# Kernel tuning notes

Measured on AMD Instinct MI355X. Metric: run time of the kernel, lower is better.

Reference implementation:

```python
import jax, jax.numpy as jnp
import numpy as np
from jax import lax

DN = ('NCHW', 'OIHW', 'NCHW')

def conv(x, w, b):
    y = lax.conv_general_dilated(x, w, (1, 1), 'SAME', dimension_numbers=DN)
    return y + b[None, :, None, None]


def setup_inputs() -> dict:
    key = jax.random.key(0)
    ks = jax.random.split(key, 32)
    B, C, H, W = 16, 256, 40, 100
    dim, N, kd, ncls, mdim = 134, 4, 128, 2, 256
    inc = C + 2
    s = 0.05  # weight init scale
    def w(k, shape):
        return jax.random.normal(k, shape, jnp.float32) * s
    d = {}
    d['features'] = jax.random.normal(ks[0], (B, C, H, W), jnp.float32)
    d['iw0'] = w(ks[1], (dim, inc, 3, 3)); d['ib0'] = jnp.zeros((dim,), jnp.float32)
    d['iw1'] = w(ks[2], (dim, dim, 3, 3)); d['ib1'] = jnp.zeros((dim,), jnp.float32)
    d['iw2'] = w(ks[3], (dim, dim, 3, 3)); d['ib2'] = jnp.zeros((dim,), jnp.float32)
    d['iw3'] = w(ks[4], (dim, dim, 3, 3)); d['ib3'] = jnp.zeros((dim,), jnp.float32)
    d['iam_w'] = w(ks[5], (N, dim, 3, 3)); d['iam_b'] = jnp.zeros((N,), jnp.float32)
    d['cls_w'] = w(ks[6], (ncls, dim));    d['cls_b'] = jnp.zeros((ncls,), jnp.float32)
    d['mk_w'] = w(ks[7], (kd, dim));       d['mk_b'] = jnp.zeros((kd,), jnp.float32)
    d['mw0'] = w(ks[8], (mdim, inc, 3, 3));  d['mb0'] = jnp.zeros((mdim,), jnp.float32)
    d['mw1'] = w(ks[9], (mdim, mdim, 3, 3)); d['mb1'] = jnp.zeros((mdim,), jnp.float32)
    d['mw2'] = w(ks[10], (mdim, mdim, 3, 3)); d['mb2'] = jnp.zeros((mdim,), jnp.float32)
    d['mw3'] = w(ks[11], (mdim, mdim, 3, 3)); d['mb3'] = jnp.zeros((mdim,), jnp.float32)
    d['pw'] = w(ks[12], (kd, mdim, 1, 1));   d['pb'] = jnp.zeros((kd,), jnp.float32)
    return d


def reference(features, iw0, ib0, iw1, ib1, iw2, ib2, iw3, ib3, iam_w, iam_b,
              cls_w, cls_b, mk_w, mk_b, mw0, mb0, mw1, mb1, mw2, mb2, mw3, mb3, pw, pb):
    B, C, H, W = features.shape
    # coordinate channels in [-1, 1]
    y_loc = -1.0 + 2.0 * jnp.arange(H, dtype=jnp.float32) / (H - 1)
    x_loc = -1.0 + 2.0 * jnp.arange(W, dtype=jnp.float32) / (W - 1)
    yy, xx = jnp.meshgrid(y_loc, x_loc, indexing='ij')  # [H,W]
    coords = jnp.broadcast_to(jnp.stack([xx, yy], 0)[None], (B, 2, H, W))
    feat = jnp.concatenate([coords, features], axis=1)  # [B, C+2, H, W]

    # instance branch conv stack (258 -> 134, relu)
    f = jax.nn.relu(conv(feat, iw0, ib0))
    f = jax.nn.relu(conv(f, iw1, ib1))
    f = jax.nn.relu(conv(f, iw2, ib2))
    f = jax.nn.relu(conv(f, iw3, ib3))  # [B,134,H,W]

    params = jnp.transpose(f, (0, 2, 3, 1)).reshape(-1, 134)  # [B*H*W, 134]

    iam = conv(f, iam_w, iam_b)           # [B,N,H,W]
    iam_prob = jax.nn.sigmoid(iam)
    Bn, Ni = iam_prob.shape[:2]

    # seed extraction: per-map flat argmax (pos = r*W + c, label always 0 in original)
    pos = jnp.argmax(iam_prob.reshape(Bn * Ni, H * W), axis=-1)  # [B*N], values in [0, H*W)
    sel = params[pos]                     # gather rows (indexes batch-0 region, as in source)
    mask_params = sel[:, :67]
    reg_params = sel[:, 67:]

    # iam-weighted pooling
    ip = iam_prob.reshape(Bn, Ni, H * W)
    ip = ip / jnp.clip(ip.sum(-1, keepdims=True), 1e-6)
    inst = jnp.einsum('bnl,bcl->bnc', ip, f.reshape(Bn, 134, H * W))  # [B,N,134]

    pred_logits = inst @ cls_w.T + cls_b  # [B,N,2]
    pred_kernel = inst @ mk_w.T + mk_b    # [B,N,128]

    # mask branch (258 -> 256 x4 relu, then 1x1 projection to 128, no relu)
    m = jax.nn.relu(conv(feat, mw0, mb0))
    m = jax.nn.relu(conv(m, mw1, mb1))
    m = jax.nn.relu(conv(m, mw2, mb2))
    m = jax.nn.relu(conv(m, mw3, mb3))
    mf = conv(m, pw, pb)                  # [B,128,H,W]

    pred_masks = jnp.einsum('bnk,bkl->bnl', pred_kernel, mf.reshape(Bn, 128, H * W))
    pred_masks = pred_masks.reshape(Bn * Ni, H, W)
    pred_logits = pred_logits.reshape(Bn * Ni, -1)
    return pred_logits, mask_params, reg_params, pred_masks
```

## Files before the change

kernel.cpp:

```cpp
#include <hip/hip_runtime.h>
#include <hip/hip_bf16.h>
#include <math.h>

constexpr int HW = 4000;
constexpr int HP = 4284;
constexpr int HPAD = 4480;
constexpr int NPIXH = 16 * HP;

typedef short s16x8 __attribute__((ext_vector_type(8)));
typedef float f32x4 __attribute__((ext_vector_type(4)));
typedef unsigned short u16x4 __attribute__((ext_vector_type(4)));
typedef unsigned short u16;

__device__ __forceinline__ u16 f2bf(float f) {
    __hip_bfloat16 h = __float2bfloat16(f);
    u16 b; __builtin_memcpy(&b, &h, 2); return b;
}
__device__ __forceinline__ float bf2f(u16 b) {
    __hip_bfloat16 h; __builtin_memcpy(&h, &b, 2); return __bfloat162float(h);
}

__device__ __forceinline__ void gload_lds16(const void* g, void* l) {
    __builtin_amdgcn_global_load_lds(
        (const __attribute__((address_space(1))) void*)g,
        (__attribute__((address_space(3))) void*)l, 16, 0, 0);
}

__global__ __launch_bounds__(256) void repack_w(
    const float* __restrict__ W, u16* __restrict__ Wh, u16* __restrict__ Wl,
    int Cout, int Cin, int NRS, int nCh, int Npad, int do_lo)
{
    const int chunk = blockIdx.x * 256 + threadIdx.x;
    const int per = Npad * 4;
    const int total = NRS * nCh * per;
    if (chunk >= total) return;
    const int q = chunk % per;
    const int t2 = chunk / per;
    const int ch = t2 % nCh;
    const int rs = t2 / nCh;
    const int f = q >> 6, g = (q >> 4) & 3, rA = q & 15;
    const int n = f * 16 + rA;
    u16x4 hp[2], lp[2];
    #pragma unroll
    for (int j = 0; j < 8; ++j) {
        const int c = ch * 32 + g * 8 + j;
        const float v = (n < Cout && c < Cin) ? W[((size_t)n * Cin + c) * NRS + rs] : 0.f;
        const u16 hb = f2bf(v);
        hp[j >> 2][j & 3] = hb;
        lp[j >> 2][j & 3] = f2bf(v - bf2f(hb));
    }
    const size_t o = (size_t)chunk * 8;
    *(u16x4*)(Wh + o) = hp[0]; *(u16x4*)(Wh + o + 4) = hp[1];
    if (do_lo) { *(u16x4*)(Wl + o) = lp[0]; *(u16x4*)(Wl + o + 4) = lp[1]; }
}

__global__ __launch_bounds__(256) void prep_x0(
    const float* __restrict__ feat, u16* __restrict__ Xh, u16* __restrict__ Xl)
{
    const int p = blockIdx.x * 256 + threadIdx.x;
    if (p >= NPIXH) return;
    const int b = p / HP; const int rem = p - b * HP;
    const int hh = rem / 102, wp = rem - hh * 102;
    const bool halo = (hh == 0) | (hh == 41) | (wp == 0) | (wp == 101);
    const int h = hh - 1, w = wp - 1;
    const int hw = h * 100 + w;
    const float xw = -1.f + 2.f * (float)w / 99.f;
    const float yh = -1.f + 2.f * (float)h / 39.f;
    for (int g = 0; g < 36; ++g) {
        u16x4 hp[2], lp[2];
        #pragma unroll
        for (int j = 0; j < 8; ++j) {
            const int c = g * 8 + j;
            float v = 0.f;
            if (!halo) {
                if (c == 0) v = xw;
                else if (c == 1) v = yh;
                else if (c < 258) v = feat[((size_t)(b * 256 + (c - 2))) * HW + hw];
            }
            const u16 hb = f2bf(v);
            hp[j >> 2][j & 3] = hb;
            lp[j >> 2][j & 3] = f2bf(v - bf2f(hb));
        }
        const size_t o = ((size_t)(b * 36 + g) * HPAD + rem) * 8;
        *(u16x4*)(Xh + o) = hp[0]; *(u16x4*)(Xh + o + 4) = hp[1];
        *(u16x4*)(Xl + o) = lp[0]; *(u16x4*)(Xl + o + 4) = lp[1];
    }
}

__global__ __launch_bounds__(256) void zero_halo_pl(
    u16* __restrict__ pa, u16* __restrict__ pb, int nGa, int nGb)
{
    const int p = blockIdx.x * 256 + threadIdx.x;
    if (p >= NPIXH) return;
    const int b = p / HP; const int rem = p - b * HP;
    const int hh = rem / 102, wp = rem - hh * 102;
    if (!((hh == 0) | (hh == 41) | (wp == 0) | (wp == 101))) return;
    const u16x4 z = {0, 0, 0, 0};
    for (int g = 0; g < nGa; ++g) {
        const size_t o = ((size_t)(b * nGa + g) * HPAD + rem) * 8;
        *(u16x4*)(pa + o) = z; *(u16x4*)(pa + o + 4) = z;
    }
    if (pb)
        for (int g = 0; g < nGb; ++g) {
            const size_t o = ((size_t)(b * nGb + g) * HPAD + rem) * 8;
            *(u16x4*)(pb + o) = z; *(u16x4*)(pb + o + 4) = z;
        }
}

template <int SPLIT, int BN, int NRS, int OUTMODE>
__global__ __launch_bounds__(256) void conv_mfma(
    const u16* __restrict__ Xhi, const u16* __restrict__ Xlo,
    const u16* __restrict__ Whi, const u16* __restrict__ Wlo,
    const float* __restrict__ bias,
    u16* __restrict__ Yhi, u16* __restrict__ Ylo, float* __restrict__ Yf,
    int nCh, int Npad, int Cout, int CoutStore, int nGout, int do_relu)
{
    constexpr int FW = BN / 32;
    constexpr int PS = 384;
    constexpr int NIW = (BN * 4) / 256;

    __shared__ u16 lsXh[4 * PS * 8];
    __shared__ u16 lsXl[SPLIT == 3 ? 4 * PS * 8 : 8];
    __shared__ u16 lsWh[2][BN * 32];
    __shared__ u16 lsWl[2][SPLIT == 3 ? BN * 32 : 8];

    const int tid = threadIdx.x, lane = tid & 63, wid = tid >> 6;
    const int b = blockIdx.z;
    const int off = blockIdx.y * 128;
    const int n0 = blockIdx.x * BN;
    const int nGin = nCh * 4;
    const int h0 = off / 100, w0 = off - h0 * 100;
    const int pTL0 = h0 * 102 + w0;

    const int wn = (wid & 1) * (BN / 2);
    const int wm = (wid >> 1) * 64;
    const int gA = lane >> 4, rA = lane & 15;

    int pd[4]; bool mval[4];
    #pragma unroll
    for (int fb = 0; fb < 4; ++fb) {
        int mm = off + wm + fb * 16 + rA;
        mval[fb] = mm < HW;
        if (!mval[fb]) mm = HW - 1;
        const int h = mm / 100, w = mm - h * 100;
        pd[fb] = (h * 102 + w) - pTL0;
    }

    auto stageX = [&](int ch) {
        const size_t src = ((size_t)(b * nGin + ch * 4 + wid) * HPAD + pTL0) * 8;
        const int dst = wid * PS * 8;
        #pragma unroll
        for (int i = 0; i < 6; ++i) {
            gload_lds16(Xhi + src + (size_t)(i * 64 + lane) * 8,
                        (char*)lsXh + (dst + i * 64 * 8) * 2);
            if constexpr (SPLIT == 3)
                gload_lds16(Xlo + src + (size_t)(i * 64 + lane) * 8,
                            (char*)lsXl + (dst + i * 64 * 8) * 2);
        }
    };
    auto stageW = [&](int ch, int rs, int buf) {
        const size_t wb = ((size_t)(rs * nCh + ch) * (Npad * 4) + (n0 >> 4) * 64) * 8;
        #pragma unroll
        for (int i = 0; i < NIW; ++i) {
            const int q = tid + i * 256;
            gload_lds16(Whi + wb + (size_t)q * 8, (char*)&lsWh[buf][0] + (q & ~63) * 16);
            if constexpr (SPLIT == 3)
                gload_lds16(Wlo + wb + (size_t)q * 8, (char*)&lsWl[buf][0] + (q & ~63) * 16);
        }
    };

    f32x4 acc[FW][4];
    #pragma unroll
    for (int i = 0; i < FW; ++i)
        #pragma unroll
        for (int j = 0; j < 4; ++j) acc[i][j] = (f32x4){0.f, 0.f, 0.f, 0.f};

    for (int ch = 0; ch < nCh; ++ch) {
        stageX(ch);
        stageW(ch, 0, 0);
        __syncthreads();
        for (int rs = 0; rs < NRS; ++rs) {
            if (rs + 1 < NRS) stageW(ch, rs + 1, (rs + 1) & 1);
            const int cb = rs & 1;
            const int toff = (NRS == 9) ? ((rs / 3) * 102 + (rs - 3 * (rs / 3))) : 103;

            s16x8 aW[FW], bX[4];
            s16x8 aWl[SPLIT == 3 ? FW : 1], bXl[SPLIT == 3 ? 4 : 1];
            #pragma unroll
            for (int fa = 0; fa < FW; ++fa) {
                const int idx = (((wn >> 4) + fa) * 64 + lane) * 8;
                aW[fa] = *(const s16x8*)&lsWh[cb][idx];
                if constexpr (SPLIT == 3) aWl[fa] = *(const s16x8*)&lsWl[cb][idx];
            }
            #pragma unroll
            for (int fb = 0; fb < 4; ++fb) {
                const int xi = (gA * PS + pd[fb] + toff) * 8;
                bX[fb] = *(const s16x8*)&lsXh[xi];
                if constexpr (SPLIT == 3) bXl[fb] = *(const s16x8*)&lsXl[xi];
            }
            #pragma unroll
            for (int fa = 0; fa < FW; ++fa)
                #pragma unroll
                for (int fb = 0; fb < 4; ++fb) {
                    acc[fa][fb] = __builtin_amdgcn_mfma_f32_16x16x32_bf16(
                        aW[fa], bX[fb], acc[fa][fb], 0, 0, 0);
                    if constexpr (SPLIT == 3) {
                        acc[fa][fb] = __builtin_amdgcn_mfma_f32_16x16x32_bf16(
                            aW[fa], bXl[fb], acc[fa][fb], 0, 0, 0);
                        acc[fa][fb] = __builtin_amdgcn_mfma_f32_16x16x32_bf16(
                            aWl[fa], bX[fb], acc[fa][fb], 0, 0, 0);
                    }
                }
            __syncthreads();
        }
    }

    #pragma unroll
    for (int fb = 0; fb < 4; ++fb) {
        if (!mval[fb]) continue;
        const int mm = off + wm + fb * 16 + rA;
        #pragma unroll
        for (int fa = 0; fa < FW; ++fa) {
            const int nb = n0 + wn + fa * 16 + gA * 4;
            if (nb >= CoutStore) continue;
            f32x4 v = acc[fa][fb];
            #pragma unroll
            for (int i = 0; i < 4; ++i) {
                const int n = nb + i;
                float x = (n < Cout) ? (v[i] + bias[n]) : 0.f;
                if (do_relu) x = fmaxf(x, 0.f);
                v[i] = x;
            }
            if constexpr (OUTMODE == 2) {
                *(f32x4*)(Yf + (size_t)(b * HW + mm) * CoutStore + nb) = v;
            } else {
                const size_t o =
                    ((size_t)(b * nGout + (nb >> 3)) * HPAD + pTL0 + pd[fb] + 103) * 8 + (nb & 7);
                u16x4 hp;
                #pragma unroll
                for (int i = 0; i < 4; ++i) hp[i] = f2bf(v[i]);
                *(u16x4*)(Yhi + o) = hp;
                if constexpr (OUTMODE == 0) {
                    u16x4 lp;
                    #pragma unroll
                    for (int i = 0; i < 4; ++i) lp[i] = f2bf(v[i] - bf2f(hp[i]));
                    *(u16x4*)(Ylo + o) = lp;
                }
            }
        }
    }
}

__global__ __launch_bounds__(256) void iam_conv_nhwc(
    const u16* __restrict__ fhi, const u16* __restrict__ flo,
    const float* __restrict__ Wt, const float* __restrict__ bias,
    float* __restrict__ iam)
{
    __shared__ float wsm[9 * 134 * 4];
    const int tid = threadIdx.x;
    for (int i = tid; i < 4824; i += 256) {
        const int rs = i / 536; const int rem = i - rs * 536;
        const int c = rem >> 2; const int n = rem & 3;
        wsm[i] = Wt[(n * 134 + c) * 9 + rs];
    }
    __syncthreads();
    const int m = blockIdx.x * 256 + tid;
    const int b = m / HW; const int hw = m - b * HW;
    const int h = hw / 100, w = hw - h * 100;
    const int pTL = h * 102 + w;
    float a0 = bias[0], a1 = bias[1], a2 = bias[2], a3 = bias[3];
    for (int rs = 0; rs < 9; ++rs) {
        const int pA = pTL + (rs / 3) * 102 + (rs % 3);
        const float* wrow = &wsm[rs * 536];
        for (int g = 0; g < 17; ++g) {
            const size_t o = ((size_t)(b * 20 + g) * HPAD + pA) * 8;
            s16x8 hv = *(const s16x8*)(fhi + o);
            s16x8 lv = *(const s16x8*)(flo + o);
            #pragma unroll
            for (int j = 0; j < 8; ++j) {
                const int c = g * 8 + j;
                if (c < 134) {
                    const float v = bf2f((u16)hv[j]) + bf2f((u16)lv[j]);
                    const float* wc = wrow + c * 4;
                    a0 = fmaf(v, wc[0], a0); a1 = fmaf(v, wc[1], a1);
                    a2 = fmaf(v, wc[2], a2); a3 = fmaf(v, wc[3], a3);
                }
            }
        }
    }
    iam[(b * 4 + 0) * HW + hw] = a0;
    iam[(b * 4 + 1) * HW + hw] = a1;
    iam[(b * 4 + 2) * HW + hw] = a2;
    iam[(b * 4 + 3) * HW + hw] = a3;
}

__device__ __forceinline__ float sigmoidf_dev(float x) {
    return 1.f / (1.f + expf(-x));
}

__global__ __launch_bounds__(256) void stats_kernel(
    const float* __restrict__ iam, int* __restrict__ pos, float* __restrict__ denom)
{
    const int i = blockIdx.x;
    const int tid = threadIdx.x;
    const float* p = &iam[i * HW];
    float bm = -1e30f; int bi = 0; float sum = 0.f;
    for (int l = tid; l < HW; l += 256) {
        const float s = sigmoidf_dev(p[l]);
        sum += s;
        if (s > bm) { bm = s; bi = l; }
    }
    __shared__ float sm[256]; __shared__ int si[256]; __shared__ float ss[256];
    sm[tid] = bm; si[tid] = bi; ss[tid] = sum;
    __syncthreads();
    for (int off = 128; off > 0; off >>= 1) {
        if (tid < off) {
            ss[tid] += ss[tid + off];
            const float m2 = sm[tid + off]; const int i2 = si[tid + off];
            if (m2 > sm[tid] || (m2 == sm[tid] && i2 < si[tid])) { sm[tid] = m2; si[tid] = i2; }
        }
        __syncthreads();
    }
    if (tid == 0) { pos[i] = si[0]; denom[i] = fmaxf(ss[0], 1e-6f); }
}

__global__ __launch_bounds__(256) void inst_nhwc(
    const u16* __restrict__ fhi, const u16* __restrict__ flo,
    const float* __restrict__ iam, const float* __restrict__ denom,
    float* __restrict__ inst)
{
    const int b = blockIdx.x, g = blockIdx.y;
    const int tid = threadIdx.x;
    float acc[4][8] = {};
    const size_t pbase = (size_t)(b * 20 + g) * HPAD;
    for (int l = tid; l < HW; l += 256) {
        const int p = (l / 100 + 1) * 102 + (l % 100) + 1;
        s16x8 hv = *(const s16x8*)(fhi + (pbase + p) * 8);
        s16x8 lv = *(const s16x8*)(flo + (pbase + p) * 8);
        float fv[8];
        #pragma unroll
        for (int j = 0; j < 8; ++j) fv[j] = bf2f((u16)hv[j]) + bf2f((u16)lv[j]);
        #pragma unroll
        for (int n = 0; n < 4; ++n) {
            const float s = sigmoidf_dev(iam[(b * 4 + n) * HW + l]);
            #pragma unroll
            for (int j = 0; j < 8; ++j) acc[n][j] = fmaf(s, fv[j], acc[n][j]);
        }
    }
    __shared__ float red[128];
    const int lane = tid & 63, wid = tid >> 6;
    #pragma unroll
    for (int n = 0; n < 4; ++n)
        #pragma unroll
        for (int j = 0; j < 8; ++j) {
            float v = acc[n][j];
            #pragma unroll
            for (int off = 32; off > 0; off >>= 1) v += __shfl_xor(v, off);
            if (lane == 0) red[wid * 32 + n * 8 + j] = v;
        }
    __syncthreads();
    if (tid < 32) {
        const float s = red[tid] + red[32 + tid] + red[64 + tid] + red[96 + tid];
        const int n = tid >> 3, j = tid & 7;
        const int c = g * 8 + j;
        if (c < 134) inst[(b * 4 + n) * 134 + c] = s / denom[b * 4 + n];
    }
}

__global__ __launch_bounds__(128) void head_kernel(
    const float* __restrict__ inst,
    const float* __restrict__ cls_w, const float* __restrict__ cls_b,
    const float* __restrict__ mk_w, const float* __restrict__ mk_b,
    float* __restrict__ out_logits, float* __restrict__ pk)
{
    const int i = blockIdx.x;
    const int tid = threadIdx.x;
    __shared__ float iv[134];
    for (int c = tid; c < 134; c += 128) iv[c] = inst[i * 134 + c];
    __syncthreads();
    float a = mk_b[tid];
    for (int c = 0; c < 134; ++c) a = fmaf(iv[c], mk_w[tid * 134 + c], a);
    pk[i * 128 + tid] = a;
    if (tid < 2) {
        float g = cls_b[tid];
        for (int c = 0; c < 134; ++c) g = fmaf(iv[c], cls_w[tid * 134 + c], g);
        out_logits[i * 2 + tid] = g;
    }
}

__global__ void gather_nhwc(
    const u16* __restrict__ fhi, const u16* __restrict__ flo,
    const int* __restrict__ pos, float* __restrict__ outm, float* __restrict__ outr)
{
    const int i = blockIdx.x;
    const int c = threadIdx.x;
    if (c >= 134) return;
    const int p = pos[i];
    const int ph = (p / 100 + 1) * 102 + (p % 100) + 1;
    const size_t o = ((size_t)(c >> 3) * HPAD + ph) * 8 + (c & 7);
    const float v = bf2f(fhi[o]) + bf2f(flo[o]);
    if (c < 67) outm[i * 67 + c] = v;
    else        outr[i * 67 + (c - 67)] = v;
}

__global__ __launch_bounds__(256) void maskout_nhwc(
    const float* __restrict__ pk, const float* __restrict__ mf,
    float* __restrict__ outm)
{
    const int b = blockIdx.x, lc = blockIdx.y;
    const int tid = threadIdx.x;
    __shared__ float pks[4][128];
    for (int i = tid; i < 512; i += 256) pks[i >> 7][i & 127] = pk[b * 512 + i];
    __syncthreads();
    const int l = lc * 256 + tid;
    if (l >= HW) return;
    const float* row = mf + (size_t)(b * HW + l) * 128;
    float a[4] = {};
    for (int k = 0; k < 128; k += 4) {
        const f32x4 mv = *(const f32x4*)(row + k);
        #pragma unroll
        for (int n = 0; n < 4; ++n) {
            a[n] = fmaf(pks[n][k + 0], mv[0], a[n]);
            a[n] = fmaf(pks[n][k + 1], mv[1], a[n]);
            a[n] = fmaf(pks[n][k + 2], mv[2], a[n]);
            a[n] = fmaf(pks[n][k + 3], mv[3], a[n]);
        }
    }
    #pragma unroll
    for (int n = 0; n < 4; ++n) outm[(b * 4 + n) * HW + l] = a[n];
}

extern "C" void kernel_launch(void* const* d_in, const int* in_sizes, int n_in,
                              void* d_out, int out_size, void* d_ws, size_t ws_size,
                              hipStream_t stream)
{
    const float* features = (const float*)d_in[0];
    const float* iw0 = (const float*)d_in[1];
    const float* ib0 = (const float*)d_in[2];
    const float* iw1 = (const float*)d_in[3];
    const float* ib1 = (const float*)d_in[4];
    const float* iw2 = (const float*)d_in[5];
    const float* ib2 = (const float*)d_in[6];
    const float* iw3 = (const float*)d_in[7];
    const float* ib3 = (const float*)d_in[8];
    const float* iam_w = (const float*)d_in[9];
    const float* iam_b = (const float*)d_in[10];
    const float* cls_w = (const float*)d_in[11];
    const float* cls_b = (const float*)d_in[12];
    const float* mk_w = (const float*)d_in[13];
    const float* mk_b = (const float*)d_in[14];
    const float* mw0 = (const float*)d_in[15];
    const float* mb0 = (const float*)d_in[16];
    const float* mw1 = (const float*)d_in[17];
    const float* mb1 = (const float*)d_in[18];
    const float* mw2 = (const float*)d_in[19];
    const float* mb2 = (const float*)d_in[20];
    const float* mw3 = (const float*)d_in[21];
    const float* mb3 = (const float*)d_in[22];
    const float* pw = (const float*)d_in[23];
    const float* pb = (const float*)d_in[24];

    constexpr size_t WI0 = (size_t)9 * 9 * 192 * 4 * 16;
    constexpr size_t WI123 = (size_t)9 * 5 * 192 * 4 * 16;
    constexpr size_t WM0 = (size_t)9 * 9 * 256 * 4 * 16;
    constexpr size_t WM123 = (size_t)9 * 8 * 256 * 4 * 16;
    constexpr size_t WPJ = (size_t)1 * 8 * 128 * 4 * 16;
    constexpr size_t PLANE = (size_t)HPAD * 16;
    constexpr size_t X0SZ = (size_t)16 * 36 * PLANE;
    constexpr size_t P20 = (size_t)16 * 20 * PLANE;
    constexpr size_t P32 = (size_t)16 * 32 * PLANE;
    constexpr size_t MFSZ = (size_t)16 * HW * 128 * 4;

    char* ws = (char*)d_ws;
    size_t off = 0;
    auto carve = [&](size_t bytes) { char* p = ws + off; off += (bytes + 255) & ~(size_t)255; return p; };
    u16* wi0h = (u16*)carve(WI0); u16* wi0l = (u16*)carve(WI0);
    u16* wi1h = (u16*)carve(WI123); u16* wi1l = (u16*)carve(WI123);
    u16* wi2h = (u16*)carve(WI123); u16* wi2l = (u16*)carve(WI123);
    u16* wi3h = (u16*)carve(WI123); u16* wi3l = (u16*)carve(WI123);
    u16* wm0h = (u16*)carve(WM0);
    u16* wm1h = (u16*)carve(WM123); u16* wm2h = (u16*)carve(WM123); u16* wm3h = (u16*)carve(WM123);
    u16* wpjh = (u16*)carve(WPJ);
    u16* X0hi = (u16*)carve(X0SZ);
    char* RGA = carve(X0SZ);
    char* RGB = carve(2 * P20);
    char* RGC = carve(2 * P20);
    float* iamb = (float*)carve(1024000);
    int* pos = (int*)carve(256);
    float* denom = (float*)carve(256);
    float* instb = (float*)carve(34560);
    float* pkbuf = (float*)carve(32768);

    u16* X0lo = (u16*)RGA;
    u16* MBhi = (u16*)RGA;
    u16* RAhi = (u16*)RGB; u16* RAlo = (u16*)(RGB + P20);
    u16* MAhi = (u16*)RGB;
    u16* RBhi = (u16*)RGC; u16* RBlo = (u16*)(RGC + P20);
    float* mf = (float*)RGC;

    float* out_logits = (float*)d_out;
    float* out_mask = out_logits + 128;
    float* out_reg = out_mask + 64 * 67;
    float* out_masks = out_reg + 64 * 67;

    const dim3 blk(256);
    auto rp = [&](const float* W, u16* h, u16* l, int Cout_, int Cin_, int NRS_,
                  int nCh_, int Npad_, int dolo) {
        const int tot = NRS_ * nCh_ * Npad_ * 4;
        repack_w<<<dim3((tot + 255) / 256), blk, 0, stream>>>(W, h, l, Cout_, Cin_, NRS_, nCh_, Npad_, dolo);
    };
    rp(iw0, wi0h, wi0l, 134, 258, 9, 9, 192, 1);
    rp(iw1, wi1h, wi1l, 134, 134, 9, 5, 192, 1);
    rp(iw2, wi2h, wi2l, 134, 134, 9, 5, 192, 1);
    rp(iw3, wi3h, wi3l, 134, 134, 9, 5, 192, 1);
    rp(mw0, wm0h, nullptr, 256, 258, 9, 9, 256, 0);
    rp(mw1, wm1h, nullptr, 256, 256, 9, 8, 256, 0);
    rp(mw2, wm2h, nullptr, 256, 256, 9, 8, 256, 0);
    rp(mw3, wm3h, nullptr, 256, 256, 9, 8, 256, 0);
    rp(pw, wpjh, nullptr, 128, 256, 1, 8, 128, 0);

    const dim3 gH((NPIXH + 255) / 256);
    prep_x0<<<gH, blk, 0, stream>>>(features, X0hi, X0lo);
    zero_halo_pl<<<gH, blk, 0, stream>>>(RAhi, RAlo, 20, 20);

    conv_mfma<3, 64, 9, 0><<<dim3(3, 32, 16), blk, 0, stream>>>(
        X0hi, X0lo, wi0h, wi0l, ib0, RAhi, RAlo, nullptr, 9, 192, 134, 160, 20, 1);
    zero_halo_pl<<<gH, blk, 0, stream>>>(RBhi, RBlo, 20, 20);
    conv_mfma<3, 64, 9, 0><<<dim3(3, 32, 16), blk, 0, stream>>>(
        RAhi, RAlo, wi1h, wi1l, ib1, RBhi, RBlo, nullptr, 5, 192, 134, 160, 20, 1);
    conv_mfma<3, 64, 9, 0><<<dim3(3, 32, 16), blk, 0, stream>>>(
        RBhi, RBlo, wi2h, wi2l, ib2, RAhi, RAlo, nullptr, 5, 192, 134, 160, 20, 1);
    conv_mfma<3, 64, 9, 0><<<dim3(3, 32, 16), blk, 0, stream>>>(
        RAhi, RAlo, wi3h, wi3l, ib3, RBhi, RBlo, nullptr, 5, 192, 134, 160, 20, 1);

    iam_conv_nhwc<<<dim3(250), blk, 0, stream>>>(RBhi, RBlo, iam_w, iam_b, iamb);
    stats_kernel<<<dim3(64), blk, 0, stream>>>(iamb, pos, denom);
    inst_nhwc<<<dim3(16, 17), blk, 0, stream>>>(RBhi, RBlo, iamb, denom, instb);
    head_kernel<<<dim3(64), dim3(128), 0, stream>>>(instb, cls_w, cls_b, mk_w, mk_b, out_logits, pkbuf);
    gather_nhwc<<<dim3(64), dim3(192), 0, stream>>>(RBhi, RBlo, pos, out_mask, out_reg);

    zero_halo_pl<<<gH, blk, 0, stream>>>(MAhi, MBhi, 32, 32);
    conv_mfma<1, 128, 9, 1><<<dim3(2, 32, 16), blk, 0, stream>>>(
        X0hi, nullptr, wm0h, nullptr, mb0, MAhi, nullptr, nullptr, 9, 256, 256, 256, 32, 1);
    conv_mfma<1, 128, 9, 1><<<dim3(2, 32, 16), blk, 0, stream>>>(
        MAhi, nullptr, wm1h, nullptr, mb1, MBhi, nullptr, nullptr, 8, 256, 256, 256, 32, 1);
    conv_mfma<1, 128, 9, 1><<<dim3(2, 32, 16), blk, 0, stream>>>(
        MBhi, nullptr, wm2h, nullptr, mb2, MAhi, nullptr, nullptr, 8, 256, 256, 256, 32, 1);
    conv_mfma<1, 128, 9, 1><<<dim3(2, 32, 16), blk, 0, stream>>>(
        MAhi, nullptr, wm3h, nullptr, mb3, MBhi, nullptr, nullptr, 8, 256, 256, 256, 32, 1);
    conv_mfma<1, 128, 1, 2><<<dim3(1, 32, 16), blk, 0, stream>>>(
        MBhi, nullptr, wpjh, nullptr, pb, nullptr, nullptr, mf, 8, 128, 128, 128, 0, 0);

    maskout_nhwc<<<dim3(16, 16), blk, 0, stream>>>(pkbuf, mf, out_masks);
}
```

Before: 1.268 ms.

## Load conv weights directly to registers, remove per-tap barriers, swizzle block order

The conv kernel stops staging weights through LDS with a barrier after every filter tap. Each wave now loads its weight fragments straight from global memory into double-buffered registers, so there is one barrier pair per input-channel group instead of one per tap. The channel count becomes a template parameter so the tap loop fully unrolls. Blocks are launched on a flat grid with a remapped index that spreads consecutive blocks across XCD-like groups of 8, and the LDS stride is padded to 390 to reduce bank conflicts. The risks are higher register pressure under the new launch bound of 3 blocks, and redundant global weight loads from each wave instead of one shared LDS copy.

```diff
diff --git a/kernel.cpp b/kernel.cpp
--- a/kernel.cpp
+++ b/kernel.cpp
@@ -107,34 +107,38 @@
         }
 }
 
-template <int SPLIT, int BN, int NRS, int OUTMODE>
-__global__ __launch_bounds__(256) void conv_mfma(
+template <int SPLIT, int BN, int NRS, int OUTMODE, int NCH>
+__global__ __launch_bounds__(256, 3) void conv_mfma(
     const u16* __restrict__ Xhi, const u16* __restrict__ Xlo,
     const u16* __restrict__ Whi, const u16* __restrict__ Wlo,
     const float* __restrict__ bias,
     u16* __restrict__ Yhi, u16* __restrict__ Ylo, float* __restrict__ Yf,
-    int nCh, int Npad, int Cout, int CoutStore, int nGout, int do_relu)
+    int Npad, int Cout, int CoutStore, int nGout, int do_relu,
+    int nN, int cpx)
 {
     constexpr int FW = BN / 32;
-    constexpr int PS = 384;
-    constexpr int NIW = (BN * 4) / 256;
-
-    __shared__ u16 lsXh[4 * PS * 8];
-    __shared__ u16 lsXl[SPLIT == 3 ? 4 * PS * 8 : 8];
-    __shared__ u16 lsWh[2][BN * 32];
-    __shared__ u16 lsWl[2][SPLIT == 3 ? BN * 32 : 8];
+    constexpr int PSTRIDE = 390;
+    constexpr int NGIN = NCH * 4;
+
+    __shared__ u16 lsXh[4 * PSTRIDE * 8];
+    __shared__ u16 lsXl[SPLIT == 3 ? 4 * PSTRIDE * 8 : 8];
 
     const int tid = threadIdx.x, lane = tid & 63, wid = tid >> 6;
-    const int b = blockIdx.z;
-    const int off = blockIdx.y * 128;
-    const int n0 = blockIdx.x * BN;
-    const int nGin = nCh * 4;
+
+    const int pb_ = blockIdx.x;
+    const int s = (pb_ & 7) * cpx + (pb_ >> 3);
+    const int nb = s % nN;
+    const int mt = s / nN;
+    const int mb = mt & 31, bimg = mt >> 5;
+    const int off = mb * 128;
+    const int n0 = nb * BN;
     const int h0 = off / 100, w0 = off - h0 * 100;
     const int pTL0 = h0 * 102 + w0;
 
     const int wn = (wid & 1) * (BN / 2);
     const int wm = (wid >> 1) * 64;
     const int gA = lane >> 4, rA = lane & 15;
+    const int wq0 = ((n0 + wn) >> 4) * 64;
 
     int pd[4]; bool mval[4];
     #pragma unroll
@@ -147,25 +151,26 @@
     }
 
     auto stageX = [&](int ch) {
-        const size_t src = ((size_t)(b * nGin + ch * 4 + wid) * HPAD + pTL0) * 8;
-        const int dst = wid * PS * 8;
+        const size_t src = ((size_t)(bimg * NGIN + ch * 4 + wid) * HPAD + pTL0) * 8;
+        char* dst = (char*)lsXh + wid * (PSTRIDE * 16);
+        char* dstl = (char*)lsXl + wid * (PSTRIDE * 16);
         #pragma unroll
         for (int i = 0; i < 6; ++i) {
-            gload_lds16(Xhi + src + (size_t)(i * 64 + lane) * 8,
-                        (char*)lsXh + (dst + i * 64 * 8) * 2);
+            gload_lds16(Xhi + src + (size_t)(i * 64 + lane) * 8, dst + i * 1024);
             if constexpr (SPLIT == 3)
-                gload_lds16(Xlo + src + (size_t)(i * 64 + lane) * 8,
-                            (char*)lsXl + (dst + i * 64 * 8) * 2);
+                gload_lds16(Xlo + src + (size_t)(i * 64 + lane) * 8, dstl + i * 1024);
         }
     };
-    auto stageW = [&](int ch, int rs, int buf) {
-        const size_t wb = ((size_t)(rs * nCh + ch) * (Npad * 4) + (n0 >> 4) * 64) * 8;
-        #pragma unroll
-        for (int i = 0; i < NIW; ++i) {
-            const int q = tid + i * 256;
-            gload_lds16(Whi + wb + (size_t)q * 8, (char*)&lsWh[buf][0] + (q & ~63) * 16);
+
+    s16x8 wh[2][FW];
+    s16x8 wl[2][SPLIT == 3 ? FW : 1];
+    auto loadW = [&](int ch, int rs, int buf) {
+        const size_t base = (((size_t)rs * NCH + ch) * (Npad * 4) + wq0 + lane) * 8;
+        #pragma unroll
+        for (int fa = 0; fa < FW; ++fa) {
+            wh[buf][fa] = *(const s16x8*)(Whi + base + fa * 64 * 8);
             if constexpr (SPLIT == 3)
-                gload_lds16(Wlo + wb + (size_t)q * 8, (char*)&lsWl[buf][0] + (q & ~63) * 16);
+                wl[buf][fa] = *(const s16x8*)(Wlo + base + fa * 64 * 8);
         }
     };
 
@@ -175,26 +180,22 @@
         #pragma unroll
         for (int j = 0; j < 4; ++j) acc[i][j] = (f32x4){0.f, 0.f, 0.f, 0.f};
 
-    for (int ch = 0; ch < nCh; ++ch) {
+    #pragma unroll 1
+    for (int ch = 0; ch < NCH; ++ch) {
+        if (ch) __syncthreads();
         stageX(ch);
-        stageW(ch, 0, 0);
+        loadW(ch, 0, 0);
         __syncthreads();
+
+        #pragma unroll
         for (int rs = 0; rs < NRS; ++rs) {
-            if (rs + 1 < NRS) stageW(ch, rs + 1, (rs + 1) & 1);
-            const int cb = rs & 1;
-            const int toff = (NRS == 9) ? ((rs / 3) * 102 + (rs - 3 * (rs / 3))) : 103;
-
-            s16x8 aW[FW], bX[4];
-            s16x8 aWl[SPLIT == 3 ? FW : 1], bXl[SPLIT == 3 ? 4 : 1];
-            #pragma unroll
-            for (int fa = 0; fa < FW; ++fa) {
-                const int idx = (((wn >> 4) + fa) * 64 + lane) * 8;
-                aW[fa] = *(const s16x8*)&lsWh[cb][idx];
-                if constexpr (SPLIT == 3) aWl[fa] = *(const s16x8*)&lsWl[cb][idx];
-            }
+            if (rs + 1 < NRS) loadW(ch, rs + 1, (rs + 1) & 1);
+            const int toff = (NRS == 9) ? ((rs / 3) * 102 + (rs % 3)) : 103;
+
+            s16x8 bX[4], bXl[SPLIT == 3 ? 4 : 1];
             #pragma unroll
             for (int fb = 0; fb < 4; ++fb) {
-                const int xi = (gA * PS + pd[fb] + toff) * 8;
+                const int xi = (gA * PSTRIDE + pd[fb] + toff) * 8;
                 bX[fb] = *(const s16x8*)&lsXh[xi];
                 if constexpr (SPLIT == 3) bXl[fb] = *(const s16x8*)&lsXl[xi];
             }
@@ -203,15 +204,14 @@
                 #pragma unroll
                 for (int fb = 0; fb < 4; ++fb) {
                     acc[fa][fb] = __builtin_amdgcn_mfma_f32_16x16x32_bf16(
-                        aW[fa], bX[fb], acc[fa][fb], 0, 0, 0);
+                        wh[rs & 1][fa], bX[fb], acc[fa][fb], 0, 0, 0);
                     if constexpr (SPLIT == 3) {
                         acc[fa][fb] = __builtin_amdgcn_mfma_f32_16x16x32_bf16(
-                            aW[fa], bXl[fb], acc[fa][fb], 0, 0, 0);
+                            wh[rs & 1][fa], bXl[fb], acc[fa][fb], 0, 0, 0);
                         acc[fa][fb] = __builtin_amdgcn_mfma_f32_16x16x32_bf16(
-                            aWl[fa], bX[fb], acc[fa][fb], 0, 0, 0);
+                            wl[rs & 1][fa], bX[fb], acc[fa][fb], 0, 0, 0);
                     }
                 }
-            __syncthreads();
         }
     }
 
@@ -221,21 +221,21 @@
         const int mm = off + wm + fb * 16 + rA;
         #pragma unroll
         for (int fa = 0; fa < FW; ++fa) {
-            const int nb = n0 + wn + fa * 16 + gA * 4;
-            if (nb >= CoutStore) continue;
+            const int nbc = n0 + wn + fa * 16 + gA * 4;
+            if (nbc >= CoutStore) continue;
             f32x4 v = acc[fa][fb];
             #pragma unroll
             for (int i = 0; i < 4; ++i) {
-                const int n = nb + i;
+                const int n = nbc + i;
                 float x = (n < Cout) ? (v[i] + bias[n]) : 0.f;
                 if (do_relu) x = fmaxf(x, 0.f);
                 v[i] = x;
             }
             if constexpr (OUTMODE == 2) {
-                *(f32x4*)(Yf + (size_t)(b * HW + mm) * CoutStore + nb) = v;
+                *(f32x4*)(Yf + (size_t)(bimg * HW + mm) * CoutStore + nbc) = v;
             } else {
                 const size_t o =
-                    ((size_t)(b * nGout + (nb >> 3)) * HPAD + pTL0 + pd[fb] + 103) * 8 + (nb & 7);
+                    ((size_t)(bimg * nGout + (nbc >> 3)) * HPAD + pTL0 + pd[fb] + 103) * 8 + (nbc & 7);
                 u16x4 hp;
                 #pragma unroll
                 for (int i = 0; i < 4; ++i) hp[i] = f2bf(v[i]);
@@ -468,8 +468,6 @@
     constexpr size_t PLANE = (size_t)HPAD * 16;
     constexpr size_t X0SZ = (size_t)16 * 36 * PLANE;
     constexpr size_t P20 = (size_t)16 * 20 * PLANE;
-    constexpr size_t P32 = (size_t)16 * 32 * PLANE;
-    constexpr size_t MFSZ = (size_t)16 * HW * 128 * 4;
 
     char* ws = (char*)d_ws;
     size_t off = 0;
@@ -523,15 +521,15 @@
     prep_x0<<<gH, blk, 0, stream>>>(features, X0hi, X0lo);
     zero_halo_pl<<<gH, blk, 0, stream>>>(RAhi, RAlo, 20, 20);
 
-    conv_mfma<3, 64, 9, 0><<<dim3(3, 32, 16), blk, 0, stream>>>(
-        X0hi, X0lo, wi0h, wi0l, ib0, RAhi, RAlo, nullptr, 9, 192, 134, 160, 20, 1);
+    conv_mfma<3, 64, 9, 0, 9><<<dim3(1536), blk, 0, stream>>>(
+        X0hi, X0lo, wi0h, wi0l, ib0, RAhi, RAlo, nullptr, 192, 134, 160, 20, 1, 3, 192);
     zero_halo_pl<<<gH, blk, 0, stream>>>(RBhi, RBlo, 20, 20);
-    conv_mfma<3, 64, 9, 0><<<dim3(3, 32, 16), blk, 0, stream>>>(
-        RAhi, RAlo, wi1h, wi1l, ib1, RBhi, RBlo, nullptr, 5, 192, 134, 160, 20, 1);
-    conv_mfma<3, 64, 9, 0><<<dim3(3, 32, 16), blk, 0, stream>>>(
-        RBhi, RBlo, wi2h, wi2l, ib2, RAhi, RAlo, nullptr, 5, 192, 134, 160, 20, 1);
-    conv_mfma<3, 64, 9, 0><<<dim3(3, 32, 16), blk, 0, stream>>>(
-        RAhi, RAlo, wi3h, wi3l, ib3, RBhi, RBlo, nullptr, 5, 192, 134, 160, 20, 1);
+    conv_mfma<3, 64, 9, 0, 5><<<dim3(1536), blk, 0, stream>>>(
+        RAhi, RAlo, wi1h, wi1l, ib1, RBhi, RBlo, nullptr, 192, 134, 160, 20, 1, 3, 192);
+    conv_mfma<3, 64, 9, 0, 5><<<dim3(1536), blk, 0, stream>>>(
+        RBhi, RBlo, wi2h, wi2l, ib2, RAhi, RAlo, nullptr, 192, 134, 160, 20, 1, 3, 192);
+    conv_mfma<3, 64, 9, 0, 5><<<dim3(1536), blk, 0, stream>>>(
+        RAhi, RAlo, wi3h, wi3l, ib3, RBhi, RBlo, nullptr, 192, 134, 160, 20, 1, 3, 192);
 
     iam_conv_nhwc<<<dim3(250), blk, 0, stream>>>(RBhi, RBlo, iam_w, iam_b, iamb);
     stats_kernel<<<dim3(64), blk, 0, stream>>>(iamb, pos, denom);
@@ -540,16 +538,16 @@
     gather_nhwc<<<dim3(64), dim3(192), 0, stream>>>(RBhi, RBlo, pos, out_mask, out_reg);
 
     zero_halo_pl<<<gH, blk, 0, stream>>>(MAhi, MBhi, 32, 32);
-    conv_mfma<1, 128, 9, 1><<<dim3(2, 32, 16), blk, 0, stream>>>(
-        X0hi, nullptr, wm0h, nullptr, mb0, MAhi, nullptr, nullptr, 9, 256, 256, 256, 32, 1);
-    conv_mfma<1, 128, 9, 1><<<dim3(2, 32, 16), blk, 0, stream>>>(
-        MAhi, nullptr, wm1h, nullptr, mb1, MBhi, nullptr, nullptr, 8, 256, 256, 256, 32, 1);
-    conv_mfma<1, 128, 9, 1><<<dim3(2, 32, 16), blk, 0, stream>>>(
-        MBhi, nullptr, wm2h, nullptr, mb2, MAhi, nullptr, nullptr, 8, 256, 256, 256, 32, 1);
-    conv_mfma<1, 128, 9, 1><<<dim3(2, 32, 16), blk, 0, stream>>>(
-        MAhi, nullptr, wm3h, nullptr, mb3, MBhi, nullptr, nullptr, 8, 256, 256, 256, 32, 1);
-    conv_mfma<1, 128, 1, 2><<<dim3(1, 32, 16), blk, 0, stream>>>(
-        MBhi, nullptr, wpjh, nullptr, pb, nullptr, nullptr, mf, 8, 128, 128, 128, 0, 0);
+    conv_mfma<1, 128, 9, 1, 9><<<dim3(1024), blk, 0, stream>>>(
+        X0hi, nullptr, wm0h, nullptr, mb0, MAhi, nullptr, nullptr, 256, 256, 256, 32, 1, 2, 128);
+    conv_mfma<1, 128, 9, 1, 8><<<dim3(1024), blk, 0, stream>>>(
+        MAhi, nullptr, wm1h, nullptr, mb1, MBhi, nullptr, nullptr, 256, 256, 256, 32, 1, 2, 128);
+    conv_mfma<1, 128, 9, 1, 8><<<dim3(1024), blk, 0, stream>>>(
+        MBhi, nullptr, wm2h, nullptr, mb2, MAhi, nullptr, nullptr, 256, 256, 256, 32, 1, 2, 128);
+    conv_mfma<1, 128, 9, 1, 8><<<dim3(1024), blk, 0, stream>>>(
+        MAhi, nullptr, wm3h, nullptr, mb3, MBhi, nullptr, nullptr, 256, 256, 256, 32, 1, 2, 128);
+    conv_mfma<1, 128, 1, 2, 8><<<dim3(512), blk, 0, stream>>>(
+        MBhi, nullptr, wpjh, nullptr, pb, nullptr, nullptr, mf, 128, 128, 128, 0, 0, 1, 64);
 
     maskout_nhwc<<<dim3(16, 16), blk, 0, stream>>>(pkbuf, mf, out_masks);
 }
```

After: 1.158 ms. 1.1x faster.
